# Kernel tuning notes

Hardware: AMD Instinct MI355X
Metric: run time of the kernel (lower is better)

## Reference

```python
import jax, jax.numpy as jnp
import numpy as np

DROPOUT_RATE = 0.25
MASK_KEY = jax.random.key(42)

def _masks(key, shape, rate):
    keep = 1.0 - rate
    k1, k2, k3 = jax.random.split(key, 3)
    m = lambda k: jax.random.bernoulli(k, keep, shape).astype(jnp.float32) / keep
    return m(k1), m(k2), m(k3)  # out_mask, h_mask, c_mask

def _lstm_layer(x, W_ih, W_hh, b_ih, b_hh, layer_key, rate):
    # x: [B, T, D]; W_ih: [4H, D]; W_hh: [4H, H]
    B, T, _ = x.shape
    H = W_hh.shape[1]
    m_out, m_h, m_c = _masks(layer_key, (B, H), rate)  # variational: shared across time
    # Precompute input-to-gate projection for the whole sequence (one big GEMM).
    xg = jnp.einsum('btd,gd->tbg', x, W_ih) + (b_ih + b_hh)  # [T, B, 4H]

    def step(carry, xg_t):
        h, c = carry
        g = xg_t + h @ W_hh.T  # [B, 4H]
        i, f, gg, o = jnp.split(g, 4, axis=-1)
        i, f, o = jax.nn.sigmoid(i), jax.nn.sigmoid(f), jax.nn.sigmoid(o)
        c = f * c + i * jnp.tanh(gg)
        h = o * jnp.tanh(c)
        out = h * m_out
        return (h * m_h, c * m_c), out

    h0 = jnp.zeros((B, H), x.dtype)
    c0 = jnp.zeros((B, H), x.dtype)
    _, ys = jax.lax.scan(step, (h0, c0), xg)  # ys: [T, B, H]
    return jnp.transpose(ys, (1, 0, 2))  # [B, T, H]

def setup_inputs() -> dict:
    key = jax.random.key(0)
    ks = jax.random.split(key, 9)
    B, T, D, H = 64, 512, 256, 256
    s_ih = 1.0 / np.sqrt(D)
    s_hh = 1.0 / np.sqrt(H)
    return {
        'x': jax.random.normal(ks[0], (B, T, D), jnp.float32),
        'W_ih0': jax.random.uniform(ks[1], (4 * H, D), jnp.float32, -s_ih, s_ih),
        'W_hh0': jax.random.uniform(ks[2], (4 * H, H), jnp.float32, -s_hh, s_hh),
        'b_ih0': jax.random.uniform(ks[3], (4 * H,), jnp.float32, -s_hh, s_hh),
        'b_hh0': jax.random.uniform(ks[4], (4 * H,), jnp.float32, -s_hh, s_hh),
        'W_ih1': jax.random.uniform(ks[5], (4 * H, H), jnp.float32, -s_hh, s_hh),
        'W_hh1': jax.random.uniform(ks[6], (4 * H, H), jnp.float32, -s_hh, s_hh),
        'b_ih1': jax.random.uniform(ks[7], (4 * H,), jnp.float32, -s_hh, s_hh),
        'b_hh1': jax.random.uniform(ks[8], (4 * H,), jnp.float32, -s_hh, s_hh),
    }

def reference(x, W_ih0, W_hh0, b_ih0, b_hh0, W_ih1, W_hh1, b_ih1, b_hh1):
    k0, k1 = jax.random.split(MASK_KEY, 2)
    x = _lstm_layer(x, W_ih0, W_hh0, b_ih0, b_hh0, k0, DROPOUT_RATE)
    x = _lstm_layer(x, W_ih1, W_hh1, b_ih1, b_hh1, k1, DROPOUT_RATE)
    return x
```

## Files before the change

### kernel.cpp

```cpp
#include <hip/hip_runtime.h>

typedef unsigned int u32;
typedef unsigned short u16;

typedef short short8 __attribute__((ext_vector_type(8)));
typedef float f32x4 __attribute__((ext_vector_type(4)));


__device__ __forceinline__ float fast_exp2(float x) {
#if __has_builtin(__builtin_amdgcn_exp2f)
  return __builtin_amdgcn_exp2f(x);
#else
  return exp2f(x);
#endif
}
__device__ __forceinline__ float fast_rcp(float x) {
#if __has_builtin(__builtin_amdgcn_rcpf)
  return __builtin_amdgcn_rcpf(x);
#else
  return 1.0f / x;
#endif
}
__device__ __forceinline__ float sigmf_(float x) {
  return fast_rcp(1.0f + fast_exp2(-1.44269504088896f * x));
}
__device__ __forceinline__ float tanhf_(float x) {
  float e = fast_exp2(2.88539008177793f * x);
  return 1.0f - 2.0f * fast_rcp(e + 1.0f);
}
__device__ __forceinline__ u16 f2bf(float x) {
  u32 u = __float_as_uint(x);
  u32 r = (u + 0x7fffu + ((u >> 16) & 1u)) >> 16;
  return (u16)r;
}

#if __has_builtin(__builtin_amdgcn_fdot2_f32_bf16)
typedef __bf16 bf16x2_t __attribute__((ext_vector_type(2)));
__device__ __forceinline__ float dot2bf(u32 w, u32 h, float acc) {
  return __builtin_amdgcn_fdot2_f32_bf16(__builtin_bit_cast(bf16x2_t, w),
                                         __builtin_bit_cast(bf16x2_t, h), acc, false);
}
#else
__device__ __forceinline__ float dot2bf(u32 w, u32 h, float acc) {
  float wl = __uint_as_float(w << 16);
  float wh = __uint_as_float(w & 0xffff0000u);
  float hl = __uint_as_float(h << 16);
  float hh = __uint_as_float(h & 0xffff0000u);
  return fmaf(wh, hh, fmaf(wl, hl, acc));
}
#endif


__device__ __forceinline__ void tf_round(u32& x0, u32& x1, int r) {
  x0 += x1;
  x1 = (x1 << r) | (x1 >> (32 - r));
  x1 ^= x0;
}
__device__ void threefry(u32 k0, u32 k1, u32 c0, u32 c1, u32& o0, u32& o1) {
  u32 k2 = k0 ^ k1 ^ 0x1BD11BDAu;
  u32 x0 = c0 + k0, x1 = c1 + k1;
  tf_round(x0, x1, 13); tf_round(x0, x1, 15); tf_round(x0, x1, 26); tf_round(x0, x1, 6);
  x0 += k1; x1 += k2 + 1u;
  tf_round(x0, x1, 17); tf_round(x0, x1, 29); tf_round(x0, x1, 16); tf_round(x0, x1, 24);
  x0 += k2; x1 += k0 + 2u;
  tf_round(x0, x1, 13); tf_round(x0, x1, 15); tf_round(x0, x1, 26); tf_round(x0, x1, 6);
  x0 += k0; x1 += k1 + 3u;
  tf_round(x0, x1, 17); tf_round(x0, x1, 29); tf_round(x0, x1, 16); tf_round(x0, x1, 24);
  x0 += k1; x1 += k2 + 4u;
  tf_round(x0, x1, 13); tf_round(x0, x1, 15); tf_round(x0, x1, 26); tf_round(x0, x1, 6);
  x0 += k2; x1 += k0 + 5u;
  o0 = x0; o1 = x1;
}

#define JAX_PARTITIONABLE 1

__global__ void masks_kernel(float* __restrict__ masks) {
  int gid = blockIdx.x * 256 + threadIdx.x;
  if (gid >= 2 * 3 * 16384) return;
  int l = gid / 49152;
  int rem = gid - l * 49152;
  int typ = rem / 16384;
  int i = rem - typ * 16384;
  u32 bits;
#if JAX_PARTITIONABLE
  u32 lk0, lk1, mk0, mk1, y0, y1;
  threefry(0u, 42u, 0u, (u32)l, lk0, lk1);
  threefry(lk0, lk1, 0u, (u32)typ, mk0, mk1);
  threefry(mk0, mk1, 0u, (u32)i, y0, y1);
  bits = y0 ^ y1;
#else
  u32 a0, a1, b0, b1;
  threefry(0u, 42u, 0u, 2u, a0, a1);
  threefry(0u, 42u, 1u, 3u, b0, b1);
  u32 lk0 = (l == 0) ? a0 : a1;
  u32 lk1 = (l == 0) ? b0 : b1;
  u32 e00, e01, e10, e11, e20, e21;
  threefry(lk0, lk1, 0u, 3u, e00, e01);
  threefry(lk0, lk1, 1u, 4u, e10, e11);
  threefry(lk0, lk1, 2u, 5u, e20, e21);
  u32 mk0 = (typ == 0) ? e00 : (typ == 1) ? e20 : e11;
  u32 mk1 = (typ == 0) ? e10 : (typ == 1) ? e01 : e21;
  u32 p = (i < 8192) ? (u32)i : (u32)(i - 8192);
  u32 y0, y1;
  threefry(mk0, mk1, p, p + 8192u, y0, y1);
  bits = (i < 8192) ? y0 : y1;
#endif
  float u = __uint_as_float((bits >> 9) | 0x3f800000u) - 1.0f;
  masks[gid] = (u < 0.75f) ? (1.0f / 0.75f) : 0.0f;
}


__global__ void conv_bf16(const float* __restrict__ src, u16* __restrict__ dst, int n) {
  int gid = blockIdx.x * 256 + threadIdx.x;
  if (gid < n) dst[gid] = f2bf(src[gid]);
}

__global__ void pack_whh(const float* __restrict__ W, u32* __restrict__ Wp, u32* __restrict__ Ws) {
  int gid = blockIdx.x * 256 + threadIdx.x;
  int p = gid >> 10;
  int row = gid & 1023;
  u32 lo = f2bf(W[row * 256 + 2 * p]);
  u32 hi = f2bf(W[row * 256 + 2 * p + 1]);
  u32 v = lo | (hi << 16);
  Wp[p * 1024 + row] = v;
  if (p >= 112) Ws[row * 16 + (p - 112)] = v;
}

__global__ void add_bias(const float* __restrict__ a, const float* __restrict__ b,
                         float* __restrict__ o, int n) {
  int gid = blockIdx.x * 256 + threadIdx.x;
  if (gid < n) o[gid] = a[gid] + b[gid];
}

__global__ __launch_bounds__(256) void gemm_xg(const u16* __restrict__ A,
                                               const u16* __restrict__ Bw,
                                               float* __restrict__ xg) {
  __shared__ uint4 Als[2048];
  __shared__ uint4 Bls[2048];
  int tid = threadIdx.x;
  int m0 = blockIdx.x * 64;
  int n0 = blockIdx.y * 64;
  {
    int row = tid >> 2, kseg = tid & 3;
    const uint4* Ag = (const uint4*)(A + (size_t)(m0 + row) * 256);
    const uint4* Bg = (const uint4*)(Bw + (size_t)(n0 + row) * 256);
#pragma unroll
    for (int uu = 0; uu < 8; ++uu) {
      int kb = kseg * 8 + uu;
      Als[kb * 64 + row] = Ag[kb];
      Bls[kb * 64 + row] = Bg[kb];
    }
  }
  __syncthreads();
  int w = tid >> 6, l = tid & 63;
  int wm = (w >> 1) * 32, wn = (w & 1) * 32;
  int lm = l & 15, q = l >> 4;
  f32x4 acc00 = {0.f, 0.f, 0.f, 0.f}, acc01 = acc00, acc10 = acc00, acc11 = acc00;
#pragma unroll
  for (int ks = 0; ks < 8; ++ks) {
    int kb = ks * 4 + q;
    short8 a0 = __builtin_bit_cast(short8, Als[kb * 64 + wm + lm]);
    short8 a1 = __builtin_bit_cast(short8, Als[kb * 64 + wm + 16 + lm]);
    short8 b0 = __builtin_bit_cast(short8, Bls[kb * 64 + wn + lm]);
    short8 b1 = __builtin_bit_cast(short8, Bls[kb * 64 + wn + 16 + lm]);
    acc00 = __builtin_amdgcn_mfma_f32_16x16x32_bf16(a0, b0, acc00, 0, 0, 0);
    acc01 = __builtin_amdgcn_mfma_f32_16x16x32_bf16(a0, b1, acc01, 0, 0, 0);
    acc10 = __builtin_amdgcn_mfma_f32_16x16x32_bf16(a1, b0, acc10, 0, 0, 0);
    acc11 = __builtin_amdgcn_mfma_f32_16x16x32_bf16(a1, b1, acc11, 0, 0, 0);
  }
#pragma unroll
  for (int fm = 0; fm < 2; ++fm)
#pragma unroll
    for (int fn = 0; fn < 2; ++fn) {
      f32x4 acc = (fm == 0) ? ((fn == 0) ? acc00 : acc01) : ((fn == 0) ? acc10 : acc11);
#pragma unroll
      for (int r = 0; r < 4; ++r) {
        int m = m0 + wm + fm * 16 + q * 4 + r;
        int n = n0 + wn + fn * 16 + lm;
        int bb = m >> 9, tt = m & 511;
        xg[(size_t)tt * 65536 + (size_t)bb * 1024 + n] = acc[r];
      }
    }
}

#define REG_P 98
#define LDS_P 14

__global__ __launch_bounds__(512) void lstm_rec(
    const u32* __restrict__ Wp,
    const uint4* __restrict__ Ws,
    const float* __restrict__ xg,
    const float* __restrict__ bias,
    const float* __restrict__ masks,
    float* __restrict__ outF,
    u16* __restrict__ outB)
{
  __shared__ u32 Wl[LDS_P * 1024];
  __shared__ float gates[1024];
  __shared__ alignas(16) u16 hbf[256];

  const int tid = threadIdx.x;
  const int b = blockIdx.x;
  const int r0 = tid, r1 = tid + 512;

  u32 wreg[2 * REG_P];
#pragma unroll
  for (int p = 0; p < REG_P; ++p) wreg[p] = Wp[p * 1024 + r0];
#pragma unroll
  for (int p = 0; p < REG_P; ++p) wreg[REG_P + p] = Wp[p * 1024 + r1];

#pragma unroll
  for (int s = 0; s < LDS_P; ++s) {
    Wl[s * 1024 + r0] = Wp[(REG_P + s) * 1024 + r0];
    Wl[s * 1024 + r1] = Wp[(REG_P + s) * 1024 + r1];
  }
  if (tid < 256) hbf[tid] = 0;

  const float bias0 = bias[r0];
  const float bias1 = bias[r1];
  float c = 0.f, m_out = 0.f, m_h = 0.f, m_c = 0.f;
  if (tid < 256) {
    m_out = masks[0 * 16384 + b * 256 + tid];
    m_h   = masks[1 * 16384 + b * 256 + tid];
    m_c   = masks[2 * 16384 + b * 256 + tid];
  }
  const uint4* Wsr0 = Ws + (size_t)r0 * 4;
  const uint4* Wsr1 = Ws + (size_t)r1 * 4;
  const float* xgb = xg + b * 1024;
  float* outFb = outF ? outF + (size_t)b * 512 * 256 : (float*)0;
  u16* outBb = outB ? outB + (size_t)b * 512 * 256 : (u16*)0;

  __syncthreads();

  for (int t = 0; t < 512; ++t) {
    float xg0 = xgb[(size_t)t * 65536 + r0];
    float xg1 = xgb[(size_t)t * 65536 + r1];
    float acc0 = bias0, acc1 = bias1;
    const uint4* h4 = (const uint4*)hbf;
#pragma unroll
    for (int s4 = 0; s4 < 4; ++s4) {
      uint4 v0 = Wsr0[s4];
      uint4 v1 = Wsr1[s4];
      uint4 hp = h4[28 + s4];
      acc0 = dot2bf(v0.x, hp.x, acc0); acc1 = dot2bf(v1.x, hp.x, acc1);
      acc0 = dot2bf(v0.y, hp.y, acc0); acc1 = dot2bf(v1.y, hp.y, acc1);
      acc0 = dot2bf(v0.z, hp.z, acc0); acc1 = dot2bf(v1.z, hp.z, acc1);
      acc0 = dot2bf(v0.w, hp.w, acc0); acc1 = dot2bf(v1.w, hp.w, acc1);
    }
#pragma unroll
    for (int qq = 0; qq < 28; ++qq) {
      uint4 hp = h4[qq];
      u32 hh[4] = {hp.x, hp.y, hp.z, hp.w};
#pragma unroll
      for (int e = 0; e < 4; ++e) {
        const int p = qq * 4 + e;
        u32 w0, w1;
        if (p < REG_P) {
          w0 = wreg[p];
          w1 = wreg[REG_P + p];
        } else {
          w0 = Wl[(p - REG_P) * 1024 + r0];
          w1 = Wl[(p - REG_P) * 1024 + r1];
        }
        acc0 = dot2bf(w0, hh[e], acc0);
        acc1 = dot2bf(w1, hh[e], acc1);
      }
    }
    acc0 += xg0;
    acc1 += xg1;
    gates[r0] = acc0;
    gates[r1] = acc1;
    __syncthreads();
    if (tid < 256) {
      float gi = gates[tid];
      float gf = gates[tid + 256];
      float gg = gates[tid + 512];
      float go = gates[tid + 768];
      float fi = sigmf_(gi), ff = sigmf_(gf), fo = sigmf_(go);
      float tg = tanhf_(gg);
      c = ff * c + fi * tg;
      float hn = fo * tanhf_(c);
      float ov = hn * m_out;
      if (outFb) outFb[t * 256 + tid] = ov;
      if (outBb) outBb[t * 256 + tid] = f2bf(ov);
      hbf[tid] = f2bf(hn * m_h);
      c *= m_c;
    }
    __syncthreads();
  }
}


extern "C" void kernel_launch(void* const* d_in, const int* in_sizes, int n_in,
                              void* d_out, int out_size, void* d_ws, size_t ws_size,
                              hipStream_t stream) {
  const float* x    = (const float*)d_in[0];
  const float* Wih0 = (const float*)d_in[1];
  const float* Whh0 = (const float*)d_in[2];
  const float* bih0 = (const float*)d_in[3];
  const float* bhh0 = (const float*)d_in[4];
  const float* Wih1 = (const float*)d_in[5];
  const float* Whh1 = (const float*)d_in[6];
  const float* bih1 = (const float*)d_in[7];
  const float* bhh1 = (const float*)d_in[8];
  float* out = (float*)d_out;

  char* w = (char*)d_ws;
  float* masks = (float*)(w + 0);
  float* biasb = (float*)(w + 393216);
  u32* Wp0     = (u32*)(w + 401408);
  u32* Wp1     = (u32*)(w + 925696);
  u32* Ws0     = (u32*)(w + 1449984);
  u32* Ws1     = (u32*)(w + 1515520);
  u16* Wih0b   = (u16*)(w + 1581056);
  u16* Wih1b   = (u16*)(w + 2105344);
  u16* xb      = (u16*)(w + 2629632);
  u16* o1b     = (u16*)(w + 19406848);
  float* xg    = (float*)(w + 36184064);

  hipLaunchKernelGGL(masks_kernel, dim3(384), dim3(256), 0, stream, masks);
  hipLaunchKernelGGL(conv_bf16, dim3(32768), dim3(256), 0, stream, x, xb, 8388608);
  hipLaunchKernelGGL(conv_bf16, dim3(1024), dim3(256), 0, stream, Wih0, Wih0b, 262144);
  hipLaunchKernelGGL(conv_bf16, dim3(1024), dim3(256), 0, stream, Wih1, Wih1b, 262144);
  hipLaunchKernelGGL(pack_whh, dim3(512), dim3(256), 0, stream, Whh0, Wp0, Ws0);
  hipLaunchKernelGGL(pack_whh, dim3(512), dim3(256), 0, stream, Whh1, Wp1, Ws1);
  hipLaunchKernelGGL(add_bias, dim3(4), dim3(256), 0, stream, bih0, bhh0, biasb, 1024);
  hipLaunchKernelGGL(add_bias, dim3(4), dim3(256), 0, stream, bih1, bhh1, biasb + 1024, 1024);

  hipLaunchKernelGGL(gemm_xg, dim3(512, 16), dim3(256), 0, stream, xb, Wih0b, xg);
  hipLaunchKernelGGL(lstm_rec, dim3(64), dim3(512), 0, stream, Wp0, (const uint4*)Ws0, xg,
                     biasb, masks, (float*)nullptr, o1b);
  hipLaunchKernelGGL(gemm_xg, dim3(512, 16), dim3(256), 0, stream, o1b, Wih1b, xg);
  hipLaunchKernelGGL(lstm_rec, dim3(64), dim3(512), 0, stream, Wp1, (const uint4*)Ws1, xg,
                     biasb + 1024, masks + 49152, out, (u16*)nullptr);
}
```

Baseline: 1.941 ms.

## Fuse both LSTM layers and layer-1 input projection into one pipelined kernel

Replaces the separate layer-0 recurrence, layer-1 GEMM and layer-1 recurrence launches with one persistent kernel of 192 blocks split into three roles. The roles pass work through global-memory flags, so the layer-1 projection and recurrence run wavefront-style behind layer 0 rather than after it finishes. This overlaps the two sequential recurrences, which were the dominant serial cost. The matvec is also split into two accumulator chains to cut the dependent-FMA latency. The risks are spin-wait overhead, cross-block memory visibility, and a deadlock if not all 192 blocks are co-resident; the bounded spin covers that last case but would then give wrong results.

```diff
diff --git a/kernel.cpp b/kernel.cpp
--- a/kernel.cpp
+++ b/kernel.cpp
@@ -132,6 +132,10 @@
   if (gid < n) o[gid] = a[gid] + b[gid];
 }
 
+__global__ void init_flags(int* __restrict__ f) {
+  f[blockIdx.x * 256 + threadIdx.x] = 0;
+}
+
 __global__ __launch_bounds__(256) void gemm_xg(const u16* __restrict__ A,
                                                const u16* __restrict__ Bw,
                                                float* __restrict__ xg) {
@@ -185,91 +189,120 @@
 
 #define REG_P 98
 #define LDS_P 14
-
-__global__ __launch_bounds__(512) void lstm_rec(
-    const u32* __restrict__ Wp,
-    const uint4* __restrict__ Ws,
-    const float* __restrict__ xg,
-    const float* __restrict__ bias,
-    const float* __restrict__ masks,
-    float* __restrict__ outF,
-    u16* __restrict__ outB)
-{
-  __shared__ u32 Wl[LDS_P * 1024];
-  __shared__ float gates[1024];
-  __shared__ alignas(16) u16 hbf[256];
-
-  const int tid = threadIdx.x;
-  const int b = blockIdx.x;
-  const int r0 = tid, r1 = tid + 512;
-
-  u32 wreg[2 * REG_P];
+#define FLAG_EVERY 4
+
+__device__ __forceinline__ void waitflag(const int* f, int want) {
+  if (__hip_atomic_load(f, __ATOMIC_RELAXED, __HIP_MEMORY_SCOPE_AGENT) >= want) return;
+  int n = 0;
+  do {
+    __builtin_amdgcn_s_sleep(2);
+    if (++n > (1 << 18)) break;
+  } while (__hip_atomic_load(f, __ATOMIC_RELAXED, __HIP_MEMORY_SCOPE_AGENT) < want);
+}
+__device__ __forceinline__ u32 gloadu(const u32* p) {
+  return __hip_atomic_load(p, __ATOMIC_RELAXED, __HIP_MEMORY_SCOPE_AGENT);
+}
+__device__ __forceinline__ float gloadf(const float* p) {
+  u32 v = __hip_atomic_load((const u32*)p, __ATOMIC_RELAXED, __HIP_MEMORY_SCOPE_AGENT);
+  return __uint_as_float(v);
+}
+
+__device__ __forceinline__ void load_weights(const u32* __restrict__ Wp,
+                                             u32* wreg, u32* Wl, int r0, int r1) {
 #pragma unroll
   for (int p = 0; p < REG_P; ++p) wreg[p] = Wp[p * 1024 + r0];
 #pragma unroll
   for (int p = 0; p < REG_P; ++p) wreg[REG_P + p] = Wp[p * 1024 + r1];
-
 #pragma unroll
   for (int s = 0; s < LDS_P; ++s) {
     Wl[s * 1024 + r0] = Wp[(REG_P + s) * 1024 + r0];
     Wl[s * 1024 + r1] = Wp[(REG_P + s) * 1024 + r1];
   }
+}
+
+__device__ __forceinline__ void matvec128(const u32* __restrict__ wreg,
+                                          const u32* __restrict__ Wl,
+                                          const uint4* __restrict__ Wsr0,
+                                          const uint4* __restrict__ Wsr1,
+                                          const u16* __restrict__ hbf,
+                                          int r0, int r1, float& acc0, float& acc1) {
+  const uint4* h4 = (const uint4*)hbf;
+  uint4 st0[4], st1[4];
+#pragma unroll
+  for (int s4 = 0; s4 < 4; ++s4) { st0[s4] = Wsr0[s4]; st1[s4] = Wsr1[s4]; }
+  float a0 = acc0, b0 = 0.f, a1 = acc1, b1 = 0.f;
+#pragma unroll
+  for (int qq = 0; qq < 14; ++qq) {
+    uint4 hp = h4[qq];
+    u32 hh[4] = {hp.x, hp.y, hp.z, hp.w};
+#pragma unroll
+    for (int e = 0; e < 4; ++e) {
+      const int p = qq * 4 + e;
+      u32 w0 = wreg[p];
+      u32 w1 = wreg[REG_P + p];
+      if (e & 1) { b0 = dot2bf(w0, hh[e], b0); b1 = dot2bf(w1, hh[e], b1); }
+      else       { a0 = dot2bf(w0, hh[e], a0); a1 = dot2bf(w1, hh[e], a1); }
+    }
+  }
+#pragma unroll
+  for (int s4 = 0; s4 < 4; ++s4) {
+    uint4 hp = h4[28 + s4];
+    a0 = dot2bf(st0[s4].x, hp.x, a0); a1 = dot2bf(st1[s4].x, hp.x, a1);
+    b0 = dot2bf(st0[s4].y, hp.y, b0); b1 = dot2bf(st1[s4].y, hp.y, b1);
+    a0 = dot2bf(st0[s4].z, hp.z, a0); a1 = dot2bf(st1[s4].z, hp.z, a1);
+    b0 = dot2bf(st0[s4].w, hp.w, b0); b1 = dot2bf(st1[s4].w, hp.w, b1);
+  }
+#pragma unroll
+  for (int qq = 14; qq < 28; ++qq) {
+    uint4 hp = h4[qq];
+    u32 hh[4] = {hp.x, hp.y, hp.z, hp.w};
+#pragma unroll
+    for (int e = 0; e < 4; ++e) {
+      const int p = qq * 4 + e;
+      u32 w0, w1;
+      if (p < REG_P) {
+        w0 = wreg[p];
+        w1 = wreg[REG_P + p];
+      } else {
+        w0 = Wl[(p - REG_P) * 1024 + r0];
+        w1 = Wl[(p - REG_P) * 1024 + r1];
+      }
+      if (e & 1) { b0 = dot2bf(w0, hh[e], b0); b1 = dot2bf(w1, hh[e], b1); }
+      else       { a0 = dot2bf(w0, hh[e], a0); a1 = dot2bf(w1, hh[e], a1); }
+    }
+  }
+  acc0 = a0 + b0;
+  acc1 = a1 + b1;
+}
+
+__device__ void rec1_body(u32* Wl, float* gates, u16* hbf,
+                          const u32* __restrict__ Wp, const uint4* __restrict__ Ws,
+                          const float* __restrict__ xg, const float* __restrict__ bias,
+                          const float* __restrict__ masks, u16* __restrict__ outB,
+                          int* flag_out, int b) {
+  const int tid = threadIdx.x;
+  const int r0 = tid, r1 = tid + 512;
+  u32 wreg[2 * REG_P];
+  load_weights(Wp, wreg, Wl, r0, r1);
   if (tid < 256) hbf[tid] = 0;
-
-  const float bias0 = bias[r0];
-  const float bias1 = bias[r1];
+  const float bias0 = bias[r0], bias1 = bias[r1];
   float c = 0.f, m_out = 0.f, m_h = 0.f, m_c = 0.f;
   if (tid < 256) {
-    m_out = masks[0 * 16384 + b * 256 + tid];
-    m_h   = masks[1 * 16384 + b * 256 + tid];
-    m_c   = masks[2 * 16384 + b * 256 + tid];
+    m_out = masks[b * 256 + tid];
+    m_h   = masks[16384 + b * 256 + tid];
+    m_c   = masks[32768 + b * 256 + tid];
   }
   const uint4* Wsr0 = Ws + (size_t)r0 * 4;
   const uint4* Wsr1 = Ws + (size_t)r1 * 4;
   const float* xgb = xg + b * 1024;
-  float* outFb = outF ? outF + (size_t)b * 512 * 256 : (float*)0;
-  u16* outBb = outB ? outB + (size_t)b * 512 * 256 : (u16*)0;
-
   __syncthreads();
-
   for (int t = 0; t < 512; ++t) {
-    float xg0 = xgb[(size_t)t * 65536 + r0];
-    float xg1 = xgb[(size_t)t * 65536 + r1];
+    float xgv0 = xgb[(size_t)t * 65536 + r0];
+    float xgv1 = xgb[(size_t)t * 65536 + r1];
     float acc0 = bias0, acc1 = bias1;
-    const uint4* h4 = (const uint4*)hbf;
-#pragma unroll
-    for (int s4 = 0; s4 < 4; ++s4) {
-      uint4 v0 = Wsr0[s4];
-      uint4 v1 = Wsr1[s4];
-      uint4 hp = h4[28 + s4];
-      acc0 = dot2bf(v0.x, hp.x, acc0); acc1 = dot2bf(v1.x, hp.x, acc1);
-      acc0 = dot2bf(v0.y, hp.y, acc0); acc1 = dot2bf(v1.y, hp.y, acc1);
-      acc0 = dot2bf(v0.z, hp.z, acc0); acc1 = dot2bf(v1.z, hp.z, acc1);
-      acc0 = dot2bf(v0.w, hp.w, acc0); acc1 = dot2bf(v1.w, hp.w, acc1);
-    }
-#pragma unroll
-    for (int qq = 0; qq < 28; ++qq) {
-      uint4 hp = h4[qq];
-      u32 hh[4] = {hp.x, hp.y, hp.z, hp.w};
-#pragma unroll
-      for (int e = 0; e < 4; ++e) {
-        const int p = qq * 4 + e;
-        u32 w0, w1;
-        if (p < REG_P) {
-          w0 = wreg[p];
-          w1 = wreg[REG_P + p];
-        } else {
-          w0 = Wl[(p - REG_P) * 1024 + r0];
-          w1 = Wl[(p - REG_P) * 1024 + r1];
-        }
-        acc0 = dot2bf(w0, hh[e], acc0);
-        acc1 = dot2bf(w1, hh[e], acc1);
-      }
-    }
-    acc0 += xg0;
-    acc1 += xg1;
-    gates[r0] = acc0;
-    gates[r1] = acc1;
+    matvec128(wreg, Wl, Wsr0, Wsr1, hbf, r0, r1, acc0, acc1);
+    gates[r0] = acc0 + xgv0;
+    gates[r1] = acc1 + xgv1;
     __syncthreads();
     if (tid < 256) {
       float gi = gates[tid];
@@ -281,12 +314,147 @@
       c = ff * c + fi * tg;
       float hn = fo * tanhf_(c);
       float ov = hn * m_out;
-      if (outFb) outFb[t * 256 + tid] = ov;
-      if (outBb) outBb[t * 256 + tid] = f2bf(ov);
+      outB[t * 256 + tid] = f2bf(ov);
       hbf[tid] = f2bf(hn * m_h);
       c *= m_c;
     }
     __syncthreads();
+    if (((t & (FLAG_EVERY - 1)) == (FLAG_EVERY - 1)) && tid == 0)
+      __hip_atomic_store(flag_out, t + 1, __ATOMIC_RELEASE, __HIP_MEMORY_SCOPE_AGENT);
+  }
+}
+
+__device__ void proj_body(u32* Wl, u16* hbf,
+                          const u32* __restrict__ Wp, const uint4* __restrict__ Ws,
+                          const u32* __restrict__ xin, const float* __restrict__ bias,
+                          float* __restrict__ xgout, int* flag_in, int* flag_out, int b) {
+  const int tid = threadIdx.x;
+  const int r0 = tid, r1 = tid + 512;
+  u32 wreg[2 * REG_P];
+  load_weights(Wp, wreg, Wl, r0, r1);
+  const float bias0 = bias[r0], bias1 = bias[r1];
+  const uint4* Wsr0 = Ws + (size_t)r0 * 4;
+  const uint4* Wsr1 = Ws + (size_t)r1 * 4;
+  float* xgb = xgout + b * 1024;
+  u32* xl = (u32*)hbf;
+  bool pf = false;
+  u32 xr = 0;
+  __syncthreads();
+  for (int t = 0; t < 512; ++t) {
+    if (!pf) {
+      waitflag(flag_in, t + 1);
+      __asm__ volatile("" ::: "memory");
+      if (tid < 128) xr = gloadu(xin + t * 128 + tid);
+    }
+    if (tid < 128) xl[tid] = xr;
+    __syncthreads();
+    float acc0 = bias0, acc1 = bias1;
+    matvec128(wreg, Wl, Wsr0, Wsr1, hbf, r0, r1, acc0, acc1);
+    xgb[(size_t)t * 65536 + r0] = acc0;
+    xgb[(size_t)t * 65536 + r1] = acc1;
+    if (t < 511) {
+      int fv = __hip_atomic_load(flag_in, __ATOMIC_RELAXED, __HIP_MEMORY_SCOPE_AGENT);
+      fv = __builtin_amdgcn_readfirstlane(fv);
+      pf = fv >= t + 2;
+      if (pf) {
+        __asm__ volatile("" ::: "memory");
+        if (tid < 128) xr = gloadu(xin + (t + 1) * 128 + tid);
+      }
+    } else {
+      pf = false;
+    }
+    __syncthreads();
+    if (((t & (FLAG_EVERY - 1)) == (FLAG_EVERY - 1)) && tid == 0)
+      __hip_atomic_store(flag_out, t + 1, __ATOMIC_RELEASE, __HIP_MEMORY_SCOPE_AGENT);
+  }
+}
+
+__device__ void rec2_body(u32* Wl, float* gates, u16* hbf,
+                          const u32* __restrict__ Wp, const uint4* __restrict__ Ws,
+                          const float* __restrict__ xg, const float* __restrict__ masks,
+                          float* __restrict__ outF, int* flag_in, int b) {
+  const int tid = threadIdx.x;
+  const int r0 = tid, r1 = tid + 512;
+  u32 wreg[2 * REG_P];
+  load_weights(Wp, wreg, Wl, r0, r1);
+  if (tid < 256) hbf[tid] = 0;
+  float c = 0.f, m_out = 0.f, m_h = 0.f, m_c = 0.f;
+  if (tid < 256) {
+    m_out = masks[b * 256 + tid];
+    m_h   = masks[16384 + b * 256 + tid];
+    m_c   = masks[32768 + b * 256 + tid];
+  }
+  const uint4* Wsr0 = Ws + (size_t)r0 * 4;
+  const uint4* Wsr1 = Ws + (size_t)r1 * 4;
+  const float* xgb = xg + b * 1024;
+  bool pf = false;
+  float pxg0 = 0.f, pxg1 = 0.f;
+  __syncthreads();
+  for (int t = 0; t < 512; ++t) {
+    if (!pf) {
+      waitflag(flag_in, t + 1);
+      __asm__ volatile("" ::: "memory");
+      pxg0 = gloadf(xgb + (size_t)t * 65536 + r0);
+      pxg1 = gloadf(xgb + (size_t)t * 65536 + r1);
+    }
+    float acc0 = 0.f, acc1 = 0.f;
+    matvec128(wreg, Wl, Wsr0, Wsr1, hbf, r0, r1, acc0, acc1);
+    gates[r0] = acc0 + pxg0;
+    gates[r1] = acc1 + pxg1;
+    if (t < 511) {
+      int fv = __hip_atomic_load(flag_in, __ATOMIC_RELAXED, __HIP_MEMORY_SCOPE_AGENT);
+      fv = __builtin_amdgcn_readfirstlane(fv);
+      pf = fv >= t + 2;
+      if (pf) {
+        __asm__ volatile("" ::: "memory");
+        pxg0 = gloadf(xgb + (size_t)(t + 1) * 65536 + r0);
+        pxg1 = gloadf(xgb + (size_t)(t + 1) * 65536 + r1);
+      }
+    } else {
+      pf = false;
+    }
+    __syncthreads();
+    if (tid < 256) {
+      float gi = gates[tid];
+      float gf = gates[tid + 256];
+      float gg = gates[tid + 512];
+      float go = gates[tid + 768];
+      float fi = sigmf_(gi), ff = sigmf_(gf), fo = sigmf_(go);
+      float tg = tanhf_(gg);
+      c = ff * c + fi * tg;
+      float hn = fo * tanhf_(c);
+      float ov = hn * m_out;
+      outF[t * 256 + tid] = ov;
+      hbf[tid] = f2bf(hn * m_h);
+      c *= m_c;
+    }
+    __syncthreads();
+  }
+}
+
+__global__ __launch_bounds__(512) void lstm_fused(
+    const u32* __restrict__ Wp0, const uint4* __restrict__ Ws0,
+    const u32* __restrict__ WpI, const uint4* __restrict__ WsI,
+    const u32* __restrict__ Wp1, const uint4* __restrict__ Ws1,
+    float* __restrict__ xg, const float* __restrict__ biasb,
+    const float* __restrict__ masks, u16* __restrict__ out1,
+    float* __restrict__ outF, int* __restrict__ flags) {
+  __shared__ u32 Wl[LDS_P * 1024];
+  __shared__ alignas(16) float gates[1024];
+  __shared__ alignas(16) u16 hbf[256];
+  const int role = blockIdx.x >> 6;
+  const int b = blockIdx.x & 63;
+  int* flag1 = flags + b * 16;
+  int* flag2 = flags + 1024 + b * 16;
+  if (role == 0) {
+    rec1_body(Wl, gates, hbf, Wp0, Ws0, xg, biasb, masks,
+              out1 + (size_t)b * 131072, flag1, b);
+  } else if (role == 1) {
+    proj_body(Wl, hbf, WpI, WsI, (const u32*)(out1 + (size_t)b * 131072),
+              biasb + 1024, xg, flag1, flag2, b);
+  } else {
+    rec2_body(Wl, gates, hbf, Wp1, Ws1, xg, masks + 49152,
+              outF + (size_t)b * 131072, flag2, b);
   }
 }
 
@@ -309,28 +477,29 @@
   float* masks = (float*)(w + 0);
   float* biasb = (float*)(w + 393216);
   u32* Wp0     = (u32*)(w + 401408);
-  u32* Wp1     = (u32*)(w + 925696);
-  u32* Ws0     = (u32*)(w + 1449984);
+  u32* Ws0     = (u32*)(w + 925696);
+  u32* Wp1     = (u32*)(w + 991232);
   u32* Ws1     = (u32*)(w + 1515520);
-  u16* Wih0b   = (u16*)(w + 1581056);
-  u16* Wih1b   = (u16*)(w + 2105344);
-  u16* xb      = (u16*)(w + 2629632);
-  u16* o1b     = (u16*)(w + 19406848);
-  float* xg    = (float*)(w + 36184064);
+  u32* WpI     = (u32*)(w + 1581056);
+  u32* WsI     = (u32*)(w + 2105344);
+  u16* Wih0b   = (u16*)(w + 2170880);
+  u16* xb      = (u16*)(w + 2695168);
+  u16* out1    = (u16*)(w + 19472384);
+  int* flags   = (int*)(w + 36249600);
+  float* xg    = (float*)(w + 36257792);
 
   hipLaunchKernelGGL(masks_kernel, dim3(384), dim3(256), 0, stream, masks);
   hipLaunchKernelGGL(conv_bf16, dim3(32768), dim3(256), 0, stream, x, xb, 8388608);
   hipLaunchKernelGGL(conv_bf16, dim3(1024), dim3(256), 0, stream, Wih0, Wih0b, 262144);
-  hipLaunchKernelGGL(conv_bf16, dim3(1024), dim3(256), 0, stream, Wih1, Wih1b, 262144);
   hipLaunchKernelGGL(pack_whh, dim3(512), dim3(256), 0, stream, Whh0, Wp0, Ws0);
   hipLaunchKernelGGL(pack_whh, dim3(512), dim3(256), 0, stream, Whh1, Wp1, Ws1);
+  hipLaunchKernelGGL(pack_whh, dim3(512), dim3(256), 0, stream, Wih1, WpI, WsI);
   hipLaunchKernelGGL(add_bias, dim3(4), dim3(256), 0, stream, bih0, bhh0, biasb, 1024);
   hipLaunchKernelGGL(add_bias, dim3(4), dim3(256), 0, stream, bih1, bhh1, biasb + 1024, 1024);
+  hipLaunchKernelGGL(init_flags, dim3(8), dim3(256), 0, stream, flags);
 
   hipLaunchKernelGGL(gemm_xg, dim3(512, 16), dim3(256), 0, stream, xb, Wih0b, xg);
-  hipLaunchKernelGGL(lstm_rec, dim3(64), dim3(512), 0, stream, Wp0, (const uint4*)Ws0, xg,
-                     biasb, masks, (float*)nullptr, o1b);
-  hipLaunchKernelGGL(gemm_xg, dim3(512, 16), dim3(256), 0, stream, o1b, Wih1b, xg);
-  hipLaunchKernelGGL(lstm_rec, dim3(64), dim3(512), 0, stream, Wp1, (const uint4*)Ws1, xg,
-                     biasb + 1024, masks + 49152, out, (u16*)nullptr);
-}
+  hipLaunchKernelGGL(lstm_fused, dim3(192), dim3(512), 0, stream,
+                     Wp0, (const uint4*)Ws0, WpI, (const uint4*)WsI,
+                     Wp1, (const uint4*)Ws1, xg, biasb, masks, out1, out, flags);
+}
```

After: 2.634 ms. 35.7% more time.

## Use MFMA for recurrent matvec with fragment-packed W_hh in registers and LDS

Applied to the files above, without the earlier changes.

Replaces the per-thread bf16 dot2 recurrent matvec with 16x16x32 bf16 MFMA instructions, using a new packing kernel that lays W_hh out as MFMA A-fragments. Most fragments are held in registers (intended partly for AGPRs) and the rest in LDS. The block shrinks to 256 threads, and every thread now does the gate math. The next step's xg values are prefetched one step ahead. Only the first of the 16 MFMA output columns is useful because the hidden vector is broadcast, so most MFMA work is wasted. The large register footprint also risks spills.

```diff
diff --git a/kernel.cpp b/kernel.cpp
--- a/kernel.cpp
+++ b/kernel.cpp
@@ -33,22 +33,6 @@
   u32 r = (u + 0x7fffu + ((u >> 16) & 1u)) >> 16;
   return (u16)r;
 }
-
-#if __has_builtin(__builtin_amdgcn_fdot2_f32_bf16)
-typedef __bf16 bf16x2_t __attribute__((ext_vector_type(2)));
-__device__ __forceinline__ float dot2bf(u32 w, u32 h, float acc) {
-  return __builtin_amdgcn_fdot2_f32_bf16(__builtin_bit_cast(bf16x2_t, w),
-                                         __builtin_bit_cast(bf16x2_t, h), acc, false);
-}
-#else
-__device__ __forceinline__ float dot2bf(u32 w, u32 h, float acc) {
-  float wl = __uint_as_float(w << 16);
-  float wh = __uint_as_float(w & 0xffff0000u);
-  float hl = __uint_as_float(h << 16);
-  float hh = __uint_as_float(h & 0xffff0000u);
-  return fmaf(wh, hh, fmaf(wl, hl, acc));
-}
-#endif
 
 
 __device__ __forceinline__ void tf_round(u32& x0, u32& x1, int r) {
@@ -115,15 +99,16 @@
   if (gid < n) dst[gid] = f2bf(src[gid]);
 }
 
-__global__ void pack_whh(const float* __restrict__ W, u32* __restrict__ Wp, u32* __restrict__ Ws) {
+__global__ void pack_wf(const float* __restrict__ W, u16* __restrict__ Wf) {
   int gid = blockIdx.x * 256 + threadIdx.x;
-  int p = gid >> 10;
-  int row = gid & 1023;
-  u32 lo = f2bf(W[row * 256 + 2 * p]);
-  u32 hi = f2bf(W[row * 256 + 2 * p + 1]);
-  u32 v = lo | (hi << 16);
-  Wp[p * 1024 + row] = v;
-  if (p >= 112) Ws[row * 16 + (p - 112)] = v;
+  int j = gid & 7;
+  int l = (gid >> 3) & 63;
+  int f = (gid >> 9) & 127;
+  int w = gid >> 16;
+  int rb = f >> 3, kc = f & 7;
+  int row = w * 256 + rb * 16 + (l & 15);
+  int col = kc * 32 + (l >> 4) * 8 + j;
+  Wf[gid] = f2bf(W[row * 256 + col]);
 }
 
 __global__ void add_bias(const float* __restrict__ a, const float* __restrict__ b,
@@ -183,99 +168,107 @@
     }
 }
 
-#define REG_P 98
-#define LDS_P 14
-
-__global__ __launch_bounds__(512) void lstm_rec(
-    const u32* __restrict__ Wp,
-    const uint4* __restrict__ Ws,
+#define NW 4
+#define F_AGPR 64
+#define F_VGPR 28
+#define F_REG  (F_AGPR + F_VGPR)
+#define F_LDS  36
+
+__global__ __launch_bounds__(256) void lstm_rec(
+    const short8* __restrict__ Wf,
     const float* __restrict__ xg,
     const float* __restrict__ bias,
     const float* __restrict__ masks,
     float* __restrict__ outF,
     u16* __restrict__ outB)
 {
-  __shared__ u32 Wl[LDS_P * 1024];
-  __shared__ float gates[1024];
+  __shared__ short8 Wlds[NW * F_LDS * 64];
+  __shared__ alignas(16) float gates[1024];
   __shared__ alignas(16) u16 hbf[256];
 
   const int tid = threadIdx.x;
+  const int w = tid >> 6, l = tid & 63;
   const int b = blockIdx.x;
-  const int r0 = tid, r1 = tid + 512;
-
-  u32 wreg[2 * REG_P];
-#pragma unroll
-  for (int p = 0; p < REG_P; ++p) wreg[p] = Wp[p * 1024 + r0];
-#pragma unroll
-  for (int p = 0; p < REG_P; ++p) wreg[REG_P + p] = Wp[p * 1024 + r1];
-
-#pragma unroll
-  for (int s = 0; s < LDS_P; ++s) {
-    Wl[s * 1024 + r0] = Wp[(REG_P + s) * 1024 + r0];
-    Wl[s * 1024 + r1] = Wp[(REG_P + s) * 1024 + r1];
-  }
-  if (tid < 256) hbf[tid] = 0;
-
-  const float bias0 = bias[r0];
-  const float bias1 = bias[r1];
-  float c = 0.f, m_out = 0.f, m_h = 0.f, m_c = 0.f;
-  if (tid < 256) {
-    m_out = masks[0 * 16384 + b * 256 + tid];
-    m_h   = masks[1 * 16384 + b * 256 + tid];
-    m_c   = masks[2 * 16384 + b * 256 + tid];
-  }
-  const uint4* Wsr0 = Ws + (size_t)r0 * 4;
-  const uint4* Wsr1 = Ws + (size_t)r1 * 4;
+  const int q = l >> 4;
+
+  const short8* Wfw = Wf + (size_t)w * 128 * 64 + l;
+  short8 fa[F_AGPR];
+  short8 fv[F_VGPR];
+#pragma unroll
+  for (int f = 0; f < F_AGPR; ++f) fa[f] = Wfw[(size_t)f * 64];
+#pragma unroll
+  for (int f = 0; f < F_VGPR; ++f) fv[f] = Wfw[(size_t)(F_AGPR + f) * 64];
+#pragma unroll
+  for (int f = 0; f < F_LDS; ++f)
+    Wlds[(w * F_LDS + f) * 64 + l] = Wfw[(size_t)(F_REG + f) * 64];
+
+  hbf[tid] = 0;
+
+  const float bias0 = bias[tid];
+  const float bias1 = bias[tid + 256];
+  const float bias2 = bias[tid + 512];
+  const float bias3 = bias[tid + 768];
+  const float m_out = masks[b * 256 + tid];
+  const float m_h   = masks[16384 + b * 256 + tid];
+  const float m_c   = masks[32768 + b * 256 + tid];
+  float c = 0.f;
+
   const float* xgb = xg + b * 1024;
   float* outFb = outF ? outF + (size_t)b * 512 * 256 : (float*)0;
   u16* outBb = outB ? outB + (size_t)b * 512 * 256 : (u16*)0;
 
+  float xgc0 = xgb[tid];
+  float xgc1 = xgb[tid + 256];
+  float xgc2 = xgb[tid + 512];
+  float xgc3 = xgb[tid + 768];
+
   __syncthreads();
 
   for (int t = 0; t < 512; ++t) {
-    float xg0 = xgb[(size_t)t * 65536 + r0];
-    float xg1 = xgb[(size_t)t * 65536 + r1];
-    float acc0 = bias0, acc1 = bias1;
-    const uint4* h4 = (const uint4*)hbf;
-#pragma unroll
-    for (int s4 = 0; s4 < 4; ++s4) {
-      uint4 v0 = Wsr0[s4];
-      uint4 v1 = Wsr1[s4];
-      uint4 hp = h4[28 + s4];
-      acc0 = dot2bf(v0.x, hp.x, acc0); acc1 = dot2bf(v1.x, hp.x, acc1);
-      acc0 = dot2bf(v0.y, hp.y, acc0); acc1 = dot2bf(v1.y, hp.y, acc1);
-      acc0 = dot2bf(v0.z, hp.z, acc0); acc1 = dot2bf(v1.z, hp.z, acc1);
-      acc0 = dot2bf(v0.w, hp.w, acc0); acc1 = dot2bf(v1.w, hp.w, acc1);
-    }
-#pragma unroll
-    for (int qq = 0; qq < 28; ++qq) {
-      uint4 hp = h4[qq];
-      u32 hh[4] = {hp.x, hp.y, hp.z, hp.w};
-#pragma unroll
-      for (int e = 0; e < 4; ++e) {
-        const int p = qq * 4 + e;
-        u32 w0, w1;
-        if (p < REG_P) {
-          w0 = wreg[p];
-          w1 = wreg[REG_P + p];
-        } else {
-          w0 = Wl[(p - REG_P) * 1024 + r0];
-          w1 = Wl[(p - REG_P) * 1024 + r1];
-        }
-        acc0 = dot2bf(w0, hh[e], acc0);
-        acc1 = dot2bf(w1, hh[e], acc1);
+    float xgn0 = 0.f, xgn1 = 0.f, xgn2 = 0.f, xgn3 = 0.f;
+    if (t < 511) {
+      const float* xn = xgb + (size_t)(t + 1) * 65536;
+      xgn0 = xn[tid];
+      xgn1 = xn[tid + 256];
+      xgn2 = xn[tid + 512];
+      xgn3 = xn[tid + 768];
+    }
+
+    short8 bf[8];
+    const short8* hv = (const short8*)hbf;
+#pragma unroll
+    for (int kc = 0; kc < 8; ++kc) bf[kc] = hv[kc * 4 + q];
+
+    f32x4 acc[16];
+#pragma unroll
+    for (int rb = 0; rb < 16; ++rb) acc[rb] = f32x4{0.f, 0.f, 0.f, 0.f};
+
+#pragma unroll
+    for (int kc = 0; kc < 8; ++kc) {
+#pragma unroll
+      for (int rb = 0; rb < 16; ++rb) {
+        const int f = rb * 8 + kc;
+        short8 af;
+        if (f < F_AGPR) af = fa[f];
+        else if (f < F_REG) af = fv[f - F_AGPR];
+        else af = Wlds[(w * F_LDS + (f - F_REG)) * 64 + l];
+        acc[rb] = __builtin_amdgcn_mfma_f32_16x16x32_bf16(af, bf[kc], acc[rb], 0, 0, 0);
       }
     }
-    acc0 += xg0;
-    acc1 += xg1;
-    gates[r0] = acc0;
-    gates[r1] = acc1;
+
+    const int cidx = l & 15;
+#pragma unroll
+    for (int rb = 0; rb < 16; ++rb) {
+      if (cidx == rb)
+        *(f32x4*)&gates[w * 256 + rb * 16 + q * 4] = acc[rb];
+    }
     __syncthreads();
-    if (tid < 256) {
-      float gi = gates[tid];
-      float gf = gates[tid + 256];
-      float gg = gates[tid + 512];
-      float go = gates[tid + 768];
+
+    {
+      float gi = gates[tid] + xgc0 + bias0;
+      float gf = gates[tid + 256] + xgc1 + bias1;
+      float gg = gates[tid + 512] + xgc2 + bias2;
+      float go = gates[tid + 768] + xgc3 + bias3;
       float fi = sigmf_(gi), ff = sigmf_(gf), fo = sigmf_(go);
       float tg = tanhf_(gg);
       c = ff * c + fi * tg;
@@ -287,6 +280,8 @@
       c *= m_c;
     }
     __syncthreads();
+
+    xgc0 = xgn0; xgc1 = xgn1; xgc2 = xgn2; xgc3 = xgn3;
   }
 }
 
@@ -308,29 +303,27 @@
   char* w = (char*)d_ws;
   float* masks = (float*)(w + 0);
   float* biasb = (float*)(w + 393216);
-  u32* Wp0     = (u32*)(w + 401408);
-  u32* Wp1     = (u32*)(w + 925696);
-  u32* Ws0     = (u32*)(w + 1449984);
-  u32* Ws1     = (u32*)(w + 1515520);
-  u16* Wih0b   = (u16*)(w + 1581056);
-  u16* Wih1b   = (u16*)(w + 2105344);
-  u16* xb      = (u16*)(w + 2629632);
-  u16* o1b     = (u16*)(w + 19406848);
-  float* xg    = (float*)(w + 36184064);
+  u16* Wf0     = (u16*)(w + 401408);
+  u16* Wf1     = (u16*)(w + 925696);
+  u16* Wih0b   = (u16*)(w + 1449984);
+  u16* Wih1b   = (u16*)(w + 1974272);
+  u16* xb      = (u16*)(w + 2498560);
+  u16* o1b     = (u16*)(w + 19275776);
+  float* xg    = (float*)(w + 36052992);
 
   hipLaunchKernelGGL(masks_kernel, dim3(384), dim3(256), 0, stream, masks);
   hipLaunchKernelGGL(conv_bf16, dim3(32768), dim3(256), 0, stream, x, xb, 8388608);
   hipLaunchKernelGGL(conv_bf16, dim3(1024), dim3(256), 0, stream, Wih0, Wih0b, 262144);
   hipLaunchKernelGGL(conv_bf16, dim3(1024), dim3(256), 0, stream, Wih1, Wih1b, 262144);
-  hipLaunchKernelGGL(pack_whh, dim3(512), dim3(256), 0, stream, Whh0, Wp0, Ws0);
-  hipLaunchKernelGGL(pack_whh, dim3(512), dim3(256), 0, stream, Whh1, Wp1, Ws1);
+  hipLaunchKernelGGL(pack_wf, dim3(1024), dim3(256), 0, stream, Whh0, Wf0);
+  hipLaunchKernelGGL(pack_wf, dim3(1024), dim3(256), 0, stream, Whh1, Wf1);
   hipLaunchKernelGGL(add_bias, dim3(4), dim3(256), 0, stream, bih0, bhh0, biasb, 1024);
   hipLaunchKernelGGL(add_bias, dim3(4), dim3(256), 0, stream, bih1, bhh1, biasb + 1024, 1024);
 
   hipLaunchKernelGGL(gemm_xg, dim3(512, 16), dim3(256), 0, stream, xb, Wih0b, xg);
-  hipLaunchKernelGGL(lstm_rec, dim3(64), dim3(512), 0, stream, Wp0, (const uint4*)Ws0, xg,
+  hipLaunchKernelGGL(lstm_rec, dim3(64), dim3(256), 0, stream, (const short8*)Wf0, xg,
                      biasb, masks, (float*)nullptr, o1b);
   hipLaunchKernelGGL(gemm_xg, dim3(512, 16), dim3(256), 0, stream, o1b, Wih1b, xg);
-  hipLaunchKernelGGL(lstm_rec, dim3(64), dim3(512), 0, stream, Wp1, (const uint4*)Ws1, xg,
+  hipLaunchKernelGGL(lstm_rec, dim3(64), dim3(256), 0, stream, (const short8*)Wf1, xg,
                      biasb + 1024, masks + 49152, out, (u16*)nullptr);
 }
```

After: 3.000 ms. 1.54x slower.

## Use 1024-thread recurrent blocks with all W_hh rows held in registers

Applied to the files above, without the earlier changes.

The recurrent LSTM kernel now runs 1024 threads per batch block, one gate row per thread, and keeps all 128 packed bf16 weight pairs in registers. This removes the LDS-resident and global-side weight slices (Ws/Wl) and their per-step loads. It also prefetches the next timestep's input projection and splits the dot product into two accumulators with scheduling barriers to shorten the dependency chain. The risk is that 128 weight registers plus temporaries at 1024 threads per block may cause spills or lower occupancy, and every thread now takes part in each block-wide barrier.

```diff
diff --git a/kernel.cpp b/kernel.cpp
--- a/kernel.cpp
+++ b/kernel.cpp
@@ -115,15 +115,13 @@
   if (gid < n) dst[gid] = f2bf(src[gid]);
 }
 
-__global__ void pack_whh(const float* __restrict__ W, u32* __restrict__ Wp, u32* __restrict__ Ws) {
+__global__ void pack_whh(const float* __restrict__ W, u32* __restrict__ Wp) {
   int gid = blockIdx.x * 256 + threadIdx.x;
   int p = gid >> 10;
   int row = gid & 1023;
   u32 lo = f2bf(W[row * 256 + 2 * p]);
   u32 hi = f2bf(W[row * 256 + 2 * p + 1]);
-  u32 v = lo | (hi << 16);
-  Wp[p * 1024 + row] = v;
-  if (p >= 112) Ws[row * 16 + (p - 112)] = v;
+  Wp[p * 1024 + row] = lo | (hi << 16);
 }
 
 __global__ void add_bias(const float* __restrict__ a, const float* __restrict__ b,
@@ -183,94 +181,67 @@
     }
 }
 
-#define REG_P 98
-#define LDS_P 14
-
-__global__ __launch_bounds__(512) void lstm_rec(
+__global__ __launch_bounds__(1024, 4) void lstm_rec(
     const u32* __restrict__ Wp,
-    const uint4* __restrict__ Ws,
     const float* __restrict__ xg,
     const float* __restrict__ bias,
     const float* __restrict__ masks,
     float* __restrict__ outF,
     u16* __restrict__ outB)
 {
-  __shared__ u32 Wl[LDS_P * 1024];
-  __shared__ float gates[1024];
+  __shared__ alignas(16) float gates[1024];
   __shared__ alignas(16) u16 hbf[256];
 
   const int tid = threadIdx.x;
   const int b = blockIdx.x;
-  const int r0 = tid, r1 = tid + 512;
-
-  u32 wreg[2 * REG_P];
-#pragma unroll
-  for (int p = 0; p < REG_P; ++p) wreg[p] = Wp[p * 1024 + r0];
-#pragma unroll
-  for (int p = 0; p < REG_P; ++p) wreg[REG_P + p] = Wp[p * 1024 + r1];
-
-#pragma unroll
-  for (int s = 0; s < LDS_P; ++s) {
-    Wl[s * 1024 + r0] = Wp[(REG_P + s) * 1024 + r0];
-    Wl[s * 1024 + r1] = Wp[(REG_P + s) * 1024 + r1];
-  }
+
+  u32 w[128];
+#pragma unroll
+  for (int p = 0; p < 128; ++p) w[p] = Wp[p * 1024 + tid];
+
   if (tid < 256) hbf[tid] = 0;
 
-  const float bias0 = bias[r0];
-  const float bias1 = bias[r1];
+  const float bias0 = bias[tid];
   float c = 0.f, m_out = 0.f, m_h = 0.f, m_c = 0.f;
   if (tid < 256) {
-    m_out = masks[0 * 16384 + b * 256 + tid];
-    m_h   = masks[1 * 16384 + b * 256 + tid];
-    m_c   = masks[2 * 16384 + b * 256 + tid];
+    m_out = masks[b * 256 + tid];
+    m_h   = masks[16384 + b * 256 + tid];
+    m_c   = masks[32768 + b * 256 + tid];
   }
-  const uint4* Wsr0 = Ws + (size_t)r0 * 4;
-  const uint4* Wsr1 = Ws + (size_t)r1 * 4;
+
   const float* xgb = xg + b * 1024;
   float* outFb = outF ? outF + (size_t)b * 512 * 256 : (float*)0;
   u16* outBb = outB ? outB + (size_t)b * 512 * 256 : (u16*)0;
 
+  float xgv = xgb[tid];
   __syncthreads();
 
   for (int t = 0; t < 512; ++t) {
-    float xg0 = xgb[(size_t)t * 65536 + r0];
-    float xg1 = xgb[(size_t)t * 65536 + r1];
-    float acc0 = bias0, acc1 = bias1;
+    float xgn = 0.f;
+    if (t < 511) xgn = xgb[(size_t)(t + 1) * 65536 + tid];
+
     const uint4* h4 = (const uint4*)hbf;
-#pragma unroll
-    for (int s4 = 0; s4 < 4; ++s4) {
-      uint4 v0 = Wsr0[s4];
-      uint4 v1 = Wsr1[s4];
-      uint4 hp = h4[28 + s4];
-      acc0 = dot2bf(v0.x, hp.x, acc0); acc1 = dot2bf(v1.x, hp.x, acc1);
-      acc0 = dot2bf(v0.y, hp.y, acc0); acc1 = dot2bf(v1.y, hp.y, acc1);
-      acc0 = dot2bf(v0.z, hp.z, acc0); acc1 = dot2bf(v1.z, hp.z, acc1);
-      acc0 = dot2bf(v0.w, hp.w, acc0); acc1 = dot2bf(v1.w, hp.w, acc1);
+    float acc0 = 0.f, acc1 = 0.f;
+#pragma unroll
+    for (int ch = 0; ch < 8; ++ch) {
+      uint4 va = h4[ch * 4 + 0];
+      uint4 vb = h4[ch * 4 + 1];
+      uint4 vc = h4[ch * 4 + 2];
+      uint4 vd = h4[ch * 4 + 3];
+      u32 hh[16] = {va.x, va.y, va.z, va.w, vb.x, vb.y, vb.z, vb.w,
+                    vc.x, vc.y, vc.z, vc.w, vd.x, vd.y, vd.z, vd.w};
+#pragma unroll
+      for (int i = 0; i < 16; ++i) {
+        const int p = ch * 16 + i;
+        if (i & 1) acc1 = dot2bf(w[p], hh[i], acc1);
+        else       acc0 = dot2bf(w[p], hh[i], acc0);
+      }
+      __builtin_amdgcn_sched_barrier(0);
     }
-#pragma unroll
-    for (int qq = 0; qq < 28; ++qq) {
-      uint4 hp = h4[qq];
-      u32 hh[4] = {hp.x, hp.y, hp.z, hp.w};
-#pragma unroll
-      for (int e = 0; e < 4; ++e) {
-        const int p = qq * 4 + e;
-        u32 w0, w1;
-        if (p < REG_P) {
-          w0 = wreg[p];
-          w1 = wreg[REG_P + p];
-        } else {
-          w0 = Wl[(p - REG_P) * 1024 + r0];
-          w1 = Wl[(p - REG_P) * 1024 + r1];
-        }
-        acc0 = dot2bf(w0, hh[e], acc0);
-        acc1 = dot2bf(w1, hh[e], acc1);
-      }
-    }
-    acc0 += xg0;
-    acc1 += xg1;
-    gates[r0] = acc0;
-    gates[r1] = acc1;
+
+    gates[tid] = acc0 + acc1 + bias0 + xgv;
     __syncthreads();
+
     if (tid < 256) {
       float gi = gates[tid];
       float gf = gates[tid + 256];
@@ -287,6 +258,8 @@
       c *= m_c;
     }
     __syncthreads();
+
+    xgv = xgn;
   }
 }
 
@@ -310,27 +283,25 @@
   float* biasb = (float*)(w + 393216);
   u32* Wp0     = (u32*)(w + 401408);
   u32* Wp1     = (u32*)(w + 925696);
-  u32* Ws0     = (u32*)(w + 1449984);
-  u32* Ws1     = (u32*)(w + 1515520);
-  u16* Wih0b   = (u16*)(w + 1581056);
-  u16* Wih1b   = (u16*)(w + 2105344);
-  u16* xb      = (u16*)(w + 2629632);
-  u16* o1b     = (u16*)(w + 19406848);
-  float* xg    = (float*)(w + 36184064);
+  u16* Wih0b   = (u16*)(w + 1449984);
+  u16* Wih1b   = (u16*)(w + 1974272);
+  u16* xb      = (u16*)(w + 2498560);
+  u16* o1b     = (u16*)(w + 19275776);
+  float* xg    = (float*)(w + 36052992);
 
   hipLaunchKernelGGL(masks_kernel, dim3(384), dim3(256), 0, stream, masks);
   hipLaunchKernelGGL(conv_bf16, dim3(32768), dim3(256), 0, stream, x, xb, 8388608);
   hipLaunchKernelGGL(conv_bf16, dim3(1024), dim3(256), 0, stream, Wih0, Wih0b, 262144);
   hipLaunchKernelGGL(conv_bf16, dim3(1024), dim3(256), 0, stream, Wih1, Wih1b, 262144);
-  hipLaunchKernelGGL(pack_whh, dim3(512), dim3(256), 0, stream, Whh0, Wp0, Ws0);
-  hipLaunchKernelGGL(pack_whh, dim3(512), dim3(256), 0, stream, Whh1, Wp1, Ws1);
+  hipLaunchKernelGGL(pack_whh, dim3(512), dim3(256), 0, stream, Whh0, Wp0);
+  hipLaunchKernelGGL(pack_whh, dim3(512), dim3(256), 0, stream, Whh1, Wp1);
   hipLaunchKernelGGL(add_bias, dim3(4), dim3(256), 0, stream, bih0, bhh0, biasb, 1024);
   hipLaunchKernelGGL(add_bias, dim3(4), dim3(256), 0, stream, bih1, bhh1, biasb + 1024, 1024);
 
   hipLaunchKernelGGL(gemm_xg, dim3(512, 16), dim3(256), 0, stream, xb, Wih0b, xg);
-  hipLaunchKernelGGL(lstm_rec, dim3(64), dim3(512), 0, stream, Wp0, (const uint4*)Ws0, xg,
+  hipLaunchKernelGGL(lstm_rec, dim3(64), dim3(1024), 0, stream, Wp0, xg,
                      biasb, masks, (float*)nullptr, o1b);
   hipLaunchKernelGGL(gemm_xg, dim3(512, 16), dim3(256), 0, stream, o1b, Wih1b, xg);
-  hipLaunchKernelGGL(lstm_rec, dim3(64), dim3(512), 0, stream, Wp1, (const uint4*)Ws1, xg,
+  hipLaunchKernelGGL(lstm_rec, dim3(64), dim3(1024), 0, stream, Wp1, xg,
                      biasb + 1024, masks + 49152, out, (u16*)nullptr);
 }
```

Result: slower. 4.658 ms (+139.9%).
